# Performance work log

Measured on AMD Instinct MI355X. Metric: run time of the kernel, lower is better.

## Reference

```python
import jax, jax.numpy as jnp
import numpy as np

N, Fdim, Aout = 8192, 32, 8
AVG_DEG = 32.0  # target average degree for the random graph


def setup_inputs() -> dict:
    key = jax.random.key(0)
    ks = jax.random.split(key, 12)
    x = jax.random.normal(ks[0], (N, Fdim), dtype=jnp.float32)
    # binary adjacency, zero diagonal (GCNConv adds self-loops itself)
    u = jax.random.uniform(ks[1], (N, N), dtype=jnp.float32)
    adj = (u < (AVG_DEG / N)).astype(jnp.float32)
    adj = adj * (1.0 - jnp.eye(N, dtype=jnp.float32))
    mask = (jax.random.uniform(ks[2], (N,), dtype=jnp.float32) < 0.5).astype(jnp.float32)

    def lin(k, fout, fin):
        s = 1.0 / np.sqrt(fin)
        return jax.random.uniform(k, (fout, fin), jnp.float32, -s, s)

    return {
        "x": x, "adj": adj, "mask": mask,
        "w1": lin(ks[3], 64, Fdim), "b1": jnp.zeros((64,), jnp.float32),
        "w2": lin(ks[4], 128, 64), "b2": jnp.zeros((128,), jnp.float32),
        "wg": lin(ks[5], 128, 128), "bg": jnp.zeros((128,), jnp.float32),
        "wd": lin(ks[6], 128, 128), "bd": jnp.zeros((128,), jnp.float32),
        "wp1": lin(ks[7], 128, 256), "bp1": jnp.zeros((128,), jnp.float32),
        "wp2": lin(ks[8], 64, 128), "bp2": jnp.zeros((64,), jnp.float32),
        "wo": lin(ks[9], Aout, 64), "bo": jnp.zeros((Aout,), jnp.float32),
    }


def reference(x, adj, mask, w1, b1, w2, b2, wg, bg, wd, bd, wp1, bp1, wp2, bp2, wo, bo):
    # encoder MLP
    h = jax.nn.relu(x @ w1.T + b1)           # [N,64]
    h = jax.nn.relu(h @ w2.T + b2)           # [N,128]
    # GCNConv with default self-loops and symmetric normalization:
    # out = D^{-1/2} (A + I) D^{-1/2} (h W^T) + b
    a_hat = adj + jnp.eye(adj.shape[0], dtype=adj.dtype)
    deg = jnp.sum(a_hat, axis=1)             # >= 1 thanks to self-loops
    dinv = jax.lax.rsqrt(deg)
    msg = h @ wg.T                            # [N,128]
    agg = dinv[:, None] * (a_hat @ (dinv[:, None] * msg))  # normalized aggregation
    g = jax.nn.relu(agg + bg)
    g = jax.nn.relu(g @ wd.T + bd)
    f = jnp.concatenate([g, h], axis=1)       # [N,256]
    p = jax.nn.relu(f @ wp1.T + bp1)
    p = jax.nn.relu(p @ wp2.T + bp2)
    out = (p @ wo.T + bo) * mask[:, None]     # [N,Aout]
    return out
```

## Files before the change

kernel.cpp:

```cpp
#include <hip/hip_runtime.h>

#define N_NODES 8192
#define CAP 128
#define ETILE 16
constexpr int AST = 132;
constexpr int WST = 129;

__global__ __launch_bounds__(256, 4) void scan_kernel(
    const float* __restrict__ adj, int* __restrict__ cnt,
    int* __restrict__ nbr, float* __restrict__ dinv) {
  const int t = threadIdx.x;
  const int lane = t & 63;
  const int row = blockIdx.x * 4 + (t >> 6);
  const uint4* rowp = (const uint4*)(adj + (size_t)row * N_NODES);
  uint4 v[8], vn[8];
#pragma unroll
  for (int i = 0; i < 8; ++i) v[i] = rowp[i * 64 + lane];
  int running = 0;
  int* nbr_row = nbr + (size_t)row * CAP;
  for (int ch = 0; ch < 4; ++ch) {
    if (ch < 3) {
      const uint4* cp = rowp + (ch + 1) * 512;
#pragma unroll
      for (int i = 0; i < 8; ++i) vn[i] = cp[i * 64 + lane];
    }
    int c = 0;
#pragma unroll
    for (int i = 0; i < 8; ++i)
      c += (v[i].x != 0u) + (v[i].y != 0u) + (v[i].z != 0u) + (v[i].w != 0u);
    int incl = c;
#pragma unroll
    for (int s = 1; s < 64; s <<= 1) {
      int n = __shfl_up(incl, s);
      if (lane >= s) incl += n;
    }
    int off = running + incl - c;
    running += __shfl(incl, 63);
    const int colbase = ch * 2048;
#pragma unroll
    for (int i = 0; i < 8; ++i) {
      if (v[i].x | v[i].y | v[i].z | v[i].w) {
        const int col = colbase + (i * 64 + lane) * 4;
        if (v[i].x) { if (off < CAP) nbr_row[off] = col + 0; ++off; }
        if (v[i].y) { if (off < CAP) nbr_row[off] = col + 1; ++off; }
        if (v[i].z) { if (off < CAP) nbr_row[off] = col + 2; ++off; }
        if (v[i].w) { if (off < CAP) nbr_row[off] = col + 3; ++off; }
      }
    }
#pragma unroll
    for (int i = 0; i < 8; ++i) v[i] = vn[i];
  }
  if (lane == 0) {
    cnt[row] = running;
    dinv[row] = rsqrtf((float)running + 1.0f);
  }
}

template <int TILE, int K, int KSPLIT, int F, bool RELU, bool BIAS, bool SCALE>
__device__ __forceinline__ void layer_op(
    const float (*__restrict__ A0)[AST], const float (*__restrict__ A1)[AST],
    float (*__restrict__ Aout)[AST], float (*__restrict__ Wb)[WST],
    const float* __restrict__ W, const float* __restrict__ bias,
    float* __restrict__ gout, const float* __restrict__ rowscale,
    int n0, int t) {
  constexpr int KC = 32;
  constexpr int NCH = K / KC;
  constexpr int ACT = (F * TILE < 256) ? F * TILE : 256;
  constexpr int RS = ACT / F;
  constexpr int RPT = TILE / RS;
  const int c = t % F;
  const int rb = t / F;
  float acc[RPT];
#pragma unroll
  for (int i = 0; i < RPT; ++i) acc[i] = 0.f;

  for (int ch = 0; ch < NCH; ++ch) {
#pragma unroll
    for (int i = 0; i < (F * KC + 255) / 256; ++i) {
      int lin = t + i * 256;
      if ((F * KC) % 256 == 0 || lin < F * KC) {
        int k = lin % KC, f = lin / KC;
        Wb[k][f] = W[(size_t)f * K + ch * KC + k];
      }
    }
    __syncthreads();
    if (t < ACT) {
      const float (*__restrict__ As)[AST] = (ch * KC < KSPLIT) ? A0 : A1;
      const int kb = (ch * KC < KSPLIT) ? ch * KC : ch * KC - KSPLIT;
#pragma unroll
      for (int kg = 0; kg < KC / 4; ++kg) {
        float w0 = Wb[kg * 4 + 0][c];
        float w1v = Wb[kg * 4 + 1][c];
        float w2v = Wb[kg * 4 + 2][c];
        float w3v = Wb[kg * 4 + 3][c];
#pragma unroll
        for (int i = 0; i < RPT; ++i) {
          const float4 a = *(const float4*)&As[rb + i * RS][kb + kg * 4];
          acc[i] = fmaf(a.x, w0, acc[i]);
          acc[i] = fmaf(a.y, w1v, acc[i]);
          acc[i] = fmaf(a.z, w2v, acc[i]);
          acc[i] = fmaf(a.w, w3v, acc[i]);
        }
      }
    }
    __syncthreads();
  }
  if (t < ACT) {
#pragma unroll
    for (int i = 0; i < RPT; ++i) {
      float v = acc[i];
      if (BIAS) v += bias[c];
      if (RELU) v = fmaxf(v, 0.f);
      int node = n0 + rb + i * RS;
      if (SCALE) v *= rowscale[node];
      if (Aout) Aout[rb + i * RS][c] = v;
      if (gout) gout[(size_t)node * F + c] = v;
    }
  }
}

__global__ __launch_bounds__(256) void encode_kernel(
    const float* __restrict__ x,
    const float* __restrict__ w1, const float* __restrict__ b1,
    const float* __restrict__ w2, const float* __restrict__ b2,
    const float* __restrict__ wg, const float* __restrict__ dinv,
    float* __restrict__ h_out, float* __restrict__ msg_out) {
  __shared__ float bufA[ETILE][AST];
  __shared__ float bufB[ETILE][AST];
  __shared__ float Wb[32][WST];
  const int t = threadIdx.x;
  const int n0 = blockIdx.x * ETILE;
  if (t < 128) {
    int row = t >> 3, k4 = (t & 7) * 4;
    *(float4*)&bufA[row][k4] = *(const float4*)&x[(size_t)(n0 + row) * 32 + k4];
  }
  layer_op<ETILE, 32, 32, 64, true, true, false>(bufA, nullptr, bufB, Wb, w1, b1, nullptr, nullptr, n0, t);
  layer_op<ETILE, 64, 64, 128, true, true, false>(bufB, nullptr, bufA, Wb, w2, b2, h_out, nullptr, n0, t);
  layer_op<ETILE, 128, 128, 128, false, false, true>(bufA, nullptr, nullptr, Wb, wg, nullptr, msg_out, dinv, n0, t);
}

__global__ __launch_bounds__(256) void agg_kernel(
    const int* __restrict__ cnt, const int* __restrict__ nbr,
    const float* __restrict__ msg, const float* __restrict__ dinv,
    const float* __restrict__ bg, const float* __restrict__ adj,
    float* __restrict__ g1) {
  const int t = threadIdx.x;
  const int f = t & 127;
  const int row = blockIdx.x * 2 + (t >> 7);
  float acc = msg[(size_t)row * 128 + f];
  const int c = cnt[row];
  if (c <= CAP) {
    int i = 0;
    for (; i + 4 <= c; i += 4) {
      int j0 = nbr[(size_t)row * CAP + i + 0];
      int j1 = nbr[(size_t)row * CAP + i + 1];
      int j2 = nbr[(size_t)row * CAP + i + 2];
      int j3 = nbr[(size_t)row * CAP + i + 3];
      float a0 = msg[(size_t)j0 * 128 + f];
      float a1 = msg[(size_t)j1 * 128 + f];
      float a2 = msg[(size_t)j2 * 128 + f];
      float a3 = msg[(size_t)j3 * 128 + f];
      acc += (a0 + a1) + (a2 + a3);
    }
    for (; i < c; ++i) {
      int j = nbr[(size_t)row * CAP + i];
      acc += msg[(size_t)j * 128 + f];
    }
  } else {
    for (int col = 0; col < N_NODES; ++col) {
      if (adj[(size_t)row * N_NODES + col] != 0.f) acc += msg[(size_t)col * 128 + f];
    }
  }
  float v = fmaf(dinv[row], acc, bg[f]);
  g1[(size_t)row * 128 + f] = fmaxf(v, 0.f);
}

__global__ __launch_bounds__(256) void decode_kernel(
    const float* __restrict__ g1, const float* __restrict__ h,
    const float* __restrict__ wd, const float* __restrict__ bd,
    const float* __restrict__ wp1, const float* __restrict__ bp1,
    const float* __restrict__ wp2, const float* __restrict__ bp2,
    const float* __restrict__ wo, const float* __restrict__ bo,
    const float* __restrict__ mask, float* __restrict__ out) {
  __shared__ float bufA[ETILE][AST];
  __shared__ float bufB[ETILE][AST];
  __shared__ float bufH[ETILE][AST];
  __shared__ float Wb[32][WST];
  const int t = threadIdx.x;
  const int n0 = blockIdx.x * ETILE;
#pragma unroll
  for (int i = 0; i < 2; ++i) {
    int lin = t + i * 256;
    int row = lin >> 5, k4 = (lin & 31) * 4;
    *(float4*)&bufA[row][k4] = *(const float4*)&g1[(size_t)(n0 + row) * 128 + k4];
    *(float4*)&bufH[row][k4] = *(const float4*)&h[(size_t)(n0 + row) * 128 + k4];
  }
  layer_op<ETILE, 128, 128, 128, true, true, false>(bufA, nullptr, bufB, Wb, wd, bd, nullptr, nullptr, n0, t);
  layer_op<ETILE, 256, 128, 128, true, true, false>(bufB, bufH, bufA, Wb, wp1, bp1, nullptr, nullptr, n0, t);
  layer_op<ETILE, 128, 128, 64, true, true, false>(bufA, nullptr, bufB, Wb, wp2, bp2, nullptr, nullptr, n0, t);
  layer_op<ETILE, 64, 64, 8, false, true, true>(bufB, nullptr, nullptr, Wb, wo, bo, out, mask, n0, t);
}

extern "C" void kernel_launch(void* const* d_in, const int* in_sizes, int n_in,
                              void* d_out, int out_size, void* d_ws, size_t ws_size,
                              hipStream_t stream) {
  const float* x    = (const float*)d_in[0];
  const float* adj  = (const float*)d_in[1];
  const float* mask = (const float*)d_in[2];
  const float* w1   = (const float*)d_in[3];
  const float* b1   = (const float*)d_in[4];
  const float* w2   = (const float*)d_in[5];
  const float* b2   = (const float*)d_in[6];
  const float* wg   = (const float*)d_in[7];
  const float* bg   = (const float*)d_in[8];
  const float* wd   = (const float*)d_in[9];
  const float* bd   = (const float*)d_in[10];
  const float* wp1  = (const float*)d_in[11];
  const float* bp1  = (const float*)d_in[12];
  const float* wp2  = (const float*)d_in[13];
  const float* bp2  = (const float*)d_in[14];
  const float* wo   = (const float*)d_in[15];
  const float* bo   = (const float*)d_in[16];
  float* out = (float*)d_out;

  float* ws = (float*)d_ws;
  float* h    = ws; ws += (size_t)N_NODES * 128;
  float* msg  = ws; ws += (size_t)N_NODES * 128;
  float* g1   = ws; ws += (size_t)N_NODES * 128;
  float* dinv = ws; ws += N_NODES;
  int* cnt = (int*)ws; ws += N_NODES;
  int* nbr = (int*)ws;

  scan_kernel<<<N_NODES / 4, 256, 0, stream>>>(adj, cnt, nbr, dinv);
  encode_kernel<<<N_NODES / ETILE, 256, 0, stream>>>(x, w1, b1, w2, b2, wg, dinv, h, msg);
  agg_kernel<<<N_NODES / 2, 256, 0, stream>>>(cnt, nbr, msg, dinv, bg, adj, g1);
  decode_kernel<<<N_NODES / ETILE, 256, 0, stream>>>(
      g1, h, wd, bd, wp1, bp1, wp2, bp2, wo, bo, mask, out);
}
```

Baseline: 468.0 us.

## Rewrite adjacency scan as grid-stride ballot compaction with atomic row counters

```diff
diff --git a/kernel.cpp b/kernel.cpp
--- a/kernel.cpp
+++ b/kernel.cpp
@@ -3,66 +3,62 @@
 #define N_NODES 8192
 #define CAP 128
 #define ETILE 16
+#define NSEG (N_NODES * N_NODES / 256)
 constexpr int AST = 132;
 constexpr int WST = 129;
 
-__global__ __launch_bounds__(256, 4) void scan_kernel(
+__global__ void zero_cnt_kernel(int* __restrict__ cnt) {
+  cnt[blockIdx.x * 256 + threadIdx.x] = 0;
+}
+
+__global__ __launch_bounds__(256, 8) void scan_kernel(
     const float* __restrict__ adj, int* __restrict__ cnt,
-    int* __restrict__ nbr, float* __restrict__ dinv) {
+    int* __restrict__ nbr) {
   const int t = threadIdx.x;
   const int lane = t & 63;
-  const int row = blockIdx.x * 4 + (t >> 6);
-  const uint4* rowp = (const uint4*)(adj + (size_t)row * N_NODES);
-  uint4 v[8], vn[8];
-#pragma unroll
-  for (int i = 0; i < 8; ++i) v[i] = rowp[i * 64 + lane];
-  int running = 0;
-  int* nbr_row = nbr + (size_t)row * CAP;
-  for (int ch = 0; ch < 4; ++ch) {
-    if (ch < 3) {
-      const uint4* cp = rowp + (ch + 1) * 512;
-#pragma unroll
-      for (int i = 0; i < 8; ++i) vn[i] = cp[i * 64 + lane];
-    }
-    int c = 0;
-#pragma unroll
-    for (int i = 0; i < 8; ++i)
-      c += (v[i].x != 0u) + (v[i].y != 0u) + (v[i].z != 0u) + (v[i].w != 0u);
-    int incl = c;
-#pragma unroll
-    for (int s = 1; s < 64; s <<= 1) {
-      int n = __shfl_up(incl, s);
-      if (lane >= s) incl += n;
-    }
-    int off = running + incl - c;
-    running += __shfl(incl, 63);
-    const int colbase = ch * 2048;
-#pragma unroll
-    for (int i = 0; i < 8; ++i) {
-      if (v[i].x | v[i].y | v[i].z | v[i].w) {
-        const int col = colbase + (i * 64 + lane) * 4;
-        if (v[i].x) { if (off < CAP) nbr_row[off] = col + 0; ++off; }
-        if (v[i].y) { if (off < CAP) nbr_row[off] = col + 1; ++off; }
-        if (v[i].z) { if (off < CAP) nbr_row[off] = col + 2; ++off; }
-        if (v[i].w) { if (off < CAP) nbr_row[off] = col + 3; ++off; }
-      }
-    }
-#pragma unroll
-    for (int i = 0; i < 8; ++i) v[i] = vn[i];
-  }
-  if (lane == 0) {
-    cnt[row] = running;
-    dinv[row] = rsqrtf((float)running + 1.0f);
-  }
-}
-
-template <int TILE, int K, int KSPLIT, int F, bool RELU, bool BIAS, bool SCALE>
+  const int nw = gridDim.x * 4;
+  const int gw = blockIdx.x * 4 + (t >> 6);
+  const unsigned long long lmask = (1ull << lane) - 1;
+  const uint4* adj4 = (const uint4*)adj;
+
+  int s = gw;
+  uint4 v = adj4[(size_t)s * 64 + lane];
+  while (s < NSEG) {
+    const int sn = s + nw;
+    uint4 vn;
+    if (sn < NSEG) vn = adj4[(size_t)sn * 64 + lane];
+    const unsigned long long m0 = __ballot(v.x != 0u);
+    const unsigned long long m1 = __ballot(v.y != 0u);
+    const unsigned long long m2 = __ballot(v.z != 0u);
+    const unsigned long long m3 = __ballot(v.w != 0u);
+    const int total = (int)(__popcll(m0) + __popcll(m1) + __popcll(m2) + __popcll(m3));
+    if (total) {
+      const int row = s >> 5;
+      const int colbase = (s & 31) * 256 + lane * 4;
+      int base;
+      if (lane == 0) base = atomicAdd(&cnt[row], total);
+      base = __shfl(base, 0);
+      int* nr = nbr + (size_t)row * CAP;
+      if (v.x != 0u) { int p = base + (int)__popcll(m0 & lmask); if (p < CAP) nr[p] = colbase + 0; }
+      base += (int)__popcll(m0);
+      if (v.y != 0u) { int p = base + (int)__popcll(m1 & lmask); if (p < CAP) nr[p] = colbase + 1; }
+      base += (int)__popcll(m1);
+      if (v.z != 0u) { int p = base + (int)__popcll(m2 & lmask); if (p < CAP) nr[p] = colbase + 2; }
+      base += (int)__popcll(m2);
+      if (v.w != 0u) { int p = base + (int)__popcll(m3 & lmask); if (p < CAP) nr[p] = colbase + 3; }
+    }
+    v = vn;
+    s = sn;
+  }
+}
+
+template <int TILE, int K, int KSPLIT, int F, bool RELU, bool BIAS, int SCALEMODE>
 __device__ __forceinline__ void layer_op(
     const float (*__restrict__ A0)[AST], const float (*__restrict__ A1)[AST],
     float (*__restrict__ Aout)[AST], float (*__restrict__ Wb)[WST],
     const float* __restrict__ W, const float* __restrict__ bias,
     float* __restrict__ gout, const float* __restrict__ rowscale,
-    int n0, int t) {
+    const int* __restrict__ degcnt, int n0, int t) {
   constexpr int KC = 32;
   constexpr int NCH = K / KC;
   constexpr int ACT = (F * TILE < 256) ? F * TILE : 256;
@@ -112,7 +108,8 @@
       if (BIAS) v += bias[c];
       if (RELU) v = fmaxf(v, 0.f);
       int node = n0 + rb + i * RS;
-      if (SCALE) v *= rowscale[node];
+      if (SCALEMODE == 1) v *= rowscale[node];
+      if (SCALEMODE == 2) v *= rsqrtf((float)degcnt[node] + 1.0f);
       if (Aout) Aout[rb + i * RS][c] = v;
       if (gout) gout[(size_t)node * F + c] = v;
     }
@@ -123,7 +120,7 @@
     const float* __restrict__ x,
     const float* __restrict__ w1, const float* __restrict__ b1,
     const float* __restrict__ w2, const float* __restrict__ b2,
-    const float* __restrict__ wg, const float* __restrict__ dinv,
+    const float* __restrict__ wg, const int* __restrict__ cnt,
     float* __restrict__ h_out, float* __restrict__ msg_out) {
   __shared__ float bufA[ETILE][AST];
   __shared__ float bufB[ETILE][AST];
@@ -134,21 +131,21 @@
     int row = t >> 3, k4 = (t & 7) * 4;
     *(float4*)&bufA[row][k4] = *(const float4*)&x[(size_t)(n0 + row) * 32 + k4];
   }
-  layer_op<ETILE, 32, 32, 64, true, true, false>(bufA, nullptr, bufB, Wb, w1, b1, nullptr, nullptr, n0, t);
-  layer_op<ETILE, 64, 64, 128, true, true, false>(bufB, nullptr, bufA, Wb, w2, b2, h_out, nullptr, n0, t);
-  layer_op<ETILE, 128, 128, 128, false, false, true>(bufA, nullptr, nullptr, Wb, wg, nullptr, msg_out, dinv, n0, t);
+  layer_op<ETILE, 32, 32, 64, true, true, 0>(bufA, nullptr, bufB, Wb, w1, b1, nullptr, nullptr, nullptr, n0, t);
+  layer_op<ETILE, 64, 64, 128, true, true, 0>(bufB, nullptr, bufA, Wb, w2, b2, h_out, nullptr, nullptr, n0, t);
+  layer_op<ETILE, 128, 128, 128, false, false, 2>(bufA, nullptr, nullptr, Wb, wg, nullptr, msg_out, nullptr, cnt, n0, t);
 }
 
 __global__ __launch_bounds__(256) void agg_kernel(
     const int* __restrict__ cnt, const int* __restrict__ nbr,
-    const float* __restrict__ msg, const float* __restrict__ dinv,
-    const float* __restrict__ bg, const float* __restrict__ adj,
-    float* __restrict__ g1) {
+    const float* __restrict__ msg, const float* __restrict__ bg,
+    const float* __restrict__ adj, float* __restrict__ g1) {
   const int t = threadIdx.x;
   const int f = t & 127;
   const int row = blockIdx.x * 2 + (t >> 7);
   float acc = msg[(size_t)row * 128 + f];
   const int c = cnt[row];
+  const float dv = rsqrtf((float)c + 1.0f);
   if (c <= CAP) {
     int i = 0;
     for (; i + 4 <= c; i += 4) {
@@ -167,11 +164,12 @@
       acc += msg[(size_t)j * 128 + f];
     }
   } else {
+    acc = msg[(size_t)row * 128 + f];
     for (int col = 0; col < N_NODES; ++col) {
       if (adj[(size_t)row * N_NODES + col] != 0.f) acc += msg[(size_t)col * 128 + f];
     }
   }
-  float v = fmaf(dinv[row], acc, bg[f]);
+  float v = fmaf(dv, acc, bg[f]);
   g1[(size_t)row * 128 + f] = fmaxf(v, 0.f);
 }
 
@@ -195,10 +193,10 @@
     *(float4*)&bufA[row][k4] = *(const float4*)&g1[(size_t)(n0 + row) * 128 + k4];
     *(float4*)&bufH[row][k4] = *(const float4*)&h[(size_t)(n0 + row) * 128 + k4];
   }
-  layer_op<ETILE, 128, 128, 128, true, true, false>(bufA, nullptr, bufB, Wb, wd, bd, nullptr, nullptr, n0, t);
-  layer_op<ETILE, 256, 128, 128, true, true, false>(bufB, bufH, bufA, Wb, wp1, bp1, nullptr, nullptr, n0, t);
-  layer_op<ETILE, 128, 128, 64, true, true, false>(bufA, nullptr, bufB, Wb, wp2, bp2, nullptr, nullptr, n0, t);
-  layer_op<ETILE, 64, 64, 8, false, true, true>(bufB, nullptr, nullptr, Wb, wo, bo, out, mask, n0, t);
+  layer_op<ETILE, 128, 128, 128, true, true, 0>(bufA, nullptr, bufB, Wb, wd, bd, nullptr, nullptr, nullptr, n0, t);
+  layer_op<ETILE, 256, 128, 128, true, true, 0>(bufB, bufH, bufA, Wb, wp1, bp1, nullptr, nullptr, nullptr, n0, t);
+  layer_op<ETILE, 128, 128, 64, true, true, 0>(bufA, nullptr, bufB, Wb, wp2, bp2, nullptr, nullptr, nullptr, n0, t);
+  layer_op<ETILE, 64, 64, 8, false, true, 1>(bufB, nullptr, nullptr, Wb, wo, bo, out, mask, nullptr, n0, t);
 }
 
 extern "C" void kernel_launch(void* const* d_in, const int* in_sizes, int n_in,
@@ -227,13 +225,13 @@
   float* h    = ws; ws += (size_t)N_NODES * 128;
   float* msg  = ws; ws += (size_t)N_NODES * 128;
   float* g1   = ws; ws += (size_t)N_NODES * 128;
-  float* dinv = ws; ws += N_NODES;
   int* cnt = (int*)ws; ws += N_NODES;
   int* nbr = (int*)ws;
 
-  scan_kernel<<<N_NODES / 4, 256, 0, stream>>>(adj, cnt, nbr, dinv);
-  encode_kernel<<<N_NODES / ETILE, 256, 0, stream>>>(x, w1, b1, w2, b2, wg, dinv, h, msg);
-  agg_kernel<<<N_NODES / 2, 256, 0, stream>>>(cnt, nbr, msg, dinv, bg, adj, g1);
+  zero_cnt_kernel<<<N_NODES / 256, 256, 0, stream>>>(cnt);
+  scan_kernel<<<2048, 256, 0, stream>>>(adj, cnt, nbr);
+  encode_kernel<<<N_NODES / ETILE, 256, 0, stream>>>(x, w1, b1, w2, b2, wg, cnt, h, msg);
+  agg_kernel<<<N_NODES / 2, 256, 0, stream>>>(cnt, nbr, msg, bg, adj, g1);
   decode_kernel<<<N_NODES / ETILE, 256, 0, stream>>>(
       g1, h, wd, bd, wp1, bp1, wp2, bp2, wo, bo, mask, out);
 }
```

New measurement: 473.4 us. No clear change (+1.2%).
